# Performance work log

Measured on AMD Instinct MI355X. Metric: run time of the kernel, lower is better.

The kernel has to match this reference:

```python
import jax, jax.numpy as jnp
import numpy as np

N, E, B = 100000, 1600000, 128
F_E, F_X, F_U, H = 128, 128, 128, 64
F_U_OUT = 128


def setup_inputs() -> dict:
    key = jax.random.key(0)
    ks = jax.random.split(key, 16)
    s = lambda fan_in: 1.0 / np.sqrt(fan_in)
    inp = {
        "x": jax.random.normal(ks[0], (N, F_X), jnp.float32),
        "e": jax.random.normal(ks[1], (E, F_E), jnp.float32),
        "u": jax.random.normal(ks[2], (B, F_U), jnp.float32),
        "edge_index": jax.random.randint(ks[3], (2, E), 0, N, jnp.int64),
        "batch": jnp.sort(jax.random.randint(ks[4], (N,), 0, B, jnp.int64)),
        # attention projection params
        "Wk_e": jax.random.uniform(ks[5], (F_E, H), jnp.float32, -s(F_E), s(F_E)),
        "bk_e": jnp.zeros((H,), jnp.float32),
        "Wq_e": jax.random.uniform(ks[6], (F_U, H), jnp.float32, -s(F_U), s(F_U)),
        "bq_e": jnp.zeros((H,), jnp.float32),
        "Wk_x": jax.random.uniform(ks[7], (F_X, H), jnp.float32, -s(F_X), s(F_X)),
        "bk_x": jnp.zeros((H,), jnp.float32),
        "Wq_x": jax.random.uniform(ks[8], (F_U, H), jnp.float32, -s(F_U), s(F_U)),
        "bq_x": jnp.zeros((H,), jnp.float32),
        # phi_u (model_fn = single Linear)
        "Wu": jax.random.uniform(ks[9], (F_E + F_X + F_U, F_U_OUT), jnp.float32,
                                  -s(F_E + F_X + F_U), s(F_E + F_X + F_U)),
        "bu": jnp.zeros((F_U_OUT,), jnp.float32),
    }
    return inp


def reference(x, e, u, edge_index, batch,
              Wk_e, bk_e, Wq_e, bq_e, Wk_x, bk_x, Wq_x, bq_x, Wu, bu):
    num_graphs = u.shape[0]
    src = edge_index[0]
    e_batch = batch[src]                       # [E] graph id per edge

    # edge attention: sigmoid(<k_e, q_e>) per edge, then scatter-add per graph
    k = e @ Wk_e + bk_e                        # [E, H]
    q = (u @ Wq_e + bq_e)[e_batch]             # [E, H] gather
    a_e = jax.nn.sigmoid(jnp.sum(k * q, axis=-1, keepdims=True))  # [E, 1]
    e_agg = jax.ops.segment_sum(a_e * e, e_batch, num_segments=num_graphs)  # [B, F_E]

    # node attention
    kx = x @ Wk_x + bk_x                       # [N, H]
    qx = (u @ Wq_x + bq_x)[batch]              # [N, H] gather
    a_x = jax.nn.sigmoid(jnp.sum(kx * qx, axis=-1, keepdims=True))  # [N, 1]
    x_agg = jax.ops.segment_sum(a_x * x, batch, num_segments=num_graphs)  # [B, F_X]

    out = jnp.concatenate([x_agg, e_agg, u], axis=1)  # [B, F_X+F_E+F_U]
    return out @ Wu + bu                        # [B, F_U_OUT]
```

## Files before the change

kernel.cpp:

```cpp
#include <hip/hip_runtime.h>
#include <hip/hip_bf16.h>


#define FDIM 128
#define BGRAPH 128
#define HDIM 64
#define SLICES 16
#define CAP 16384
#define CURSOR_STRIDE 16
#define SC_THREADS 512
#define SC_ITEMS 16

typedef float vf4 __attribute__((ext_vector_type(4)));

__device__ inline vf4 ldnt4(const float* p) {
    return __builtin_nontemporal_load(reinterpret_cast<const vf4*>(p));
}

__global__ __launch_bounds__(SC_THREADS) void prep_kernel(
    const int* __restrict__ src, const int* __restrict__ batch,
    int* __restrict__ cursor,
    int* __restrict__ order,
    float* __restrict__ e_agg,
    const float* __restrict__ u,
    const float* __restrict__ Wk_e, const float* __restrict__ bk_e,
    const float* __restrict__ Wq_e, const float* __restrict__ bq_e,
    const float* __restrict__ Wk_x, const float* __restrict__ bk_x,
    const float* __restrict__ Wq_x, const float* __restrict__ bq_x,
    float* __restrict__ v_e, float* __restrict__ v_x,
    float* __restrict__ c_e, float* __restrict__ c_x,
    int E, int nb_edge)
{
    const int t = threadIdx.x;

    if (blockIdx.x < nb_edge) {
        __shared__ int lh[BGRAPH];
        __shared__ int s_base[BGRAPH];
        if (t < BGRAPH) lh[t] = 0;
        __syncthreads();

        const int base0 = blockIdx.x * SC_THREADS * SC_ITEMS;
        int gv[SC_ITEMS], rv[SC_ITEMS];
#pragma unroll
        for (int k = 0; k < SC_ITEMS; ++k) {
            const int i = base0 + k * SC_THREADS + t;
            if (i < E) {
                const int g = batch[__builtin_nontemporal_load(src + i)];
                gv[k] = g;
                rv[k] = atomicAdd(&lh[g], 1);
            } else {
                gv[k] = -1; rv[k] = 0;
            }
        }
        __syncthreads();
        if (t < BGRAPH) {
            const int n = lh[t];
            const int b = (n > 0) ? atomicAdd(&cursor[t * CURSOR_STRIDE], n) : 0;
            s_base[t] = t * CAP + b;
        }
        __syncthreads();
#pragma unroll
        for (int k = 0; k < SC_ITEMS; ++k) {
            const int i = base0 + k * SC_THREADS + t;
            if (gv[k] >= 0) order[s_base[gv[k]] + rv[k]] = i;
        }
    } else {
        const int g = blockIdx.x - nb_edge;
        __shared__ float su[FDIM];
        __shared__ float sqe[HDIM];
        __shared__ float sqx[HDIM];

        if (t < FDIM) {
            e_agg[g * FDIM + t] = 0.f;
            su[t] = u[g * FDIM + t];
        }
        __syncthreads();

        if (t < HDIM) {
            float acc = bq_e[t];
            for (int f = 0; f < FDIM; ++f) acc += su[f] * Wq_e[f * HDIM + t];
            sqe[t] = acc;
        } else if (t < 2 * HDIM) {
            const int h = t - HDIM;
            float acc = bq_x[h];
            for (int f = 0; f < FDIM; ++f) acc += su[f] * Wq_x[f * HDIM + h];
            sqx[h] = acc;
        }
        __syncthreads();

        if (t < FDIM) {
            float acce = 0.f, accx = 0.f;
            for (int h = 0; h < HDIM; ++h) {
                acce += Wk_e[t * HDIM + h] * sqe[h];
                accx += Wk_x[t * HDIM + h] * sqx[h];
            }
            v_e[g * FDIM + t] = acce;
            v_x[g * FDIM + t] = accx;
        }
        if (t == 0) {
            float ce = 0.f, cx = 0.f;
            for (int h = 0; h < HDIM; ++h) { ce += bk_e[h] * sqe[h]; cx += bk_x[h] * sqx[h]; }
            c_e[g] = ce;
            c_x[g] = cx;
        }
    }
}

__global__ __launch_bounds__(1024) void agg_kernel(
    const float* __restrict__ e,
    const float* __restrict__ x,
    const int*   __restrict__ order,
    const int*   __restrict__ cursor,
    const int*   __restrict__ batch,
    const float* __restrict__ v_e, const float* __restrict__ c_e,
    const float* __restrict__ v_x, const float* __restrict__ c_x,
    float* __restrict__ e_agg,
    float* __restrict__ x_agg,
    int N)
{
    const int tid  = threadIdx.x;
    const int hidx = tid >> 5;
    const int hl   = tid & 31;
    __shared__ float s_red[32][FDIM];

    const int NEDGE = BGRAPH * SLICES;
    if (blockIdx.x < NEDGE) {
        const int g = blockIdx.x / SLICES;
        const int s = blockIdx.x % SLICES;
        const int len = cursor[g * CURSOR_STRIDE];
        const int lo = g * CAP;
        const int chunk = (len + SLICES - 1) / SLICES;
        const int clo = lo + s * chunk;
        const int chi = min(clo + chunk, lo + len);

        const vf4 fv = *reinterpret_cast<const vf4*>(v_e + g * FDIM + 4 * hl);
        const float cg = c_e[g];

        vf4 acc = (vf4)(0.f);

        int pos = clo + hidx;
        int j1 = 0, j2 = 0;
        vf4 fe0 = (vf4)(0.f), fe1 = (vf4)(0.f);
        if (pos < chi) {
            const int j0 = order[pos];
            fe0 = ldnt4(e + (size_t)j0 * FDIM + 4 * hl);
        }
        if (pos + 32 < chi) {
            j1 = order[pos + 32];
            fe1 = ldnt4(e + (size_t)j1 * FDIM + 4 * hl);
        }
        if (pos + 64 < chi) j2 = order[pos + 64];

        for (; pos < chi; pos += 32) {
            const int j3 = (pos + 96 < chi) ? order[pos + 96] : 0;
            vf4 fe2 = (vf4)(0.f);
            if (pos + 64 < chi)
                fe2 = ldnt4(e + (size_t)j2 * FDIM + 4 * hl);

            float d = fe0.x * fv.x + fe0.y * fv.y + fe0.z * fv.z + fe0.w * fv.w;
            d += __shfl_xor(d, 1);
            d += __shfl_xor(d, 2);
            d += __shfl_xor(d, 4);
            d += __shfl_xor(d, 8);
            d += __shfl_xor(d, 16);
            const float a = 1.f / (1.f + __expf(-(d + cg)));
            acc.x += a * fe0.x; acc.y += a * fe0.y; acc.z += a * fe0.z; acc.w += a * fe0.w;

            fe0 = fe1; fe1 = fe2; j2 = j3;
        }

        s_red[hidx][4 * hl + 0] = acc.x;
        s_red[hidx][4 * hl + 1] = acc.y;
        s_red[hidx][4 * hl + 2] = acc.z;
        s_red[hidx][4 * hl + 3] = acc.w;
        __syncthreads();

        if (tid < FDIM) {
            float ssum = 0.f;
#pragma unroll
            for (int k = 0; k < 32; ++k) ssum += s_red[k][tid];
            unsafeAtomicAdd(&e_agg[g * FDIM + tid], ssum);
        }
    } else {
        const int g = blockIdx.x - NEDGE;
        int lo = 0, hi = N;
        while (lo < hi) { int mid = (lo + hi) >> 1; if (batch[mid] < g) lo = mid + 1; else hi = mid; }
        const int start = lo;
        hi = N;
        while (lo < hi) { int mid = (lo + hi) >> 1; if (batch[mid] < g + 1) lo = mid + 1; else hi = mid; }
        const int end = lo;

        const vf4 fv = *reinterpret_cast<const vf4*>(v_x + g * FDIM + 4 * hl);
        const float cg = c_x[g];

        vf4 acc = (vf4)(0.f);
        for (int row = start + hidx; row < end; row += 32) {
            const vf4 fe = ldnt4(x + (size_t)row * FDIM + 4 * hl);
            float d = fe.x * fv.x + fe.y * fv.y + fe.z * fv.z + fe.w * fv.w;
            d += __shfl_xor(d, 1);
            d += __shfl_xor(d, 2);
            d += __shfl_xor(d, 4);
            d += __shfl_xor(d, 8);
            d += __shfl_xor(d, 16);
            const float a = 1.f / (1.f + __expf(-(d + cg)));
            acc.x += a * fe.x; acc.y += a * fe.y; acc.z += a * fe.z; acc.w += a * fe.w;
        }

        s_red[hidx][4 * hl + 0] = acc.x;
        s_red[hidx][4 * hl + 1] = acc.y;
        s_red[hidx][4 * hl + 2] = acc.z;
        s_red[hidx][4 * hl + 3] = acc.w;
        __syncthreads();

        if (tid < FDIM) {
            float ssum = 0.f;
#pragma unroll
            for (int k = 0; k < 32; ++k) ssum += s_red[k][tid];
            x_agg[g * FDIM + tid] = ssum;
        }
    }
}

__global__ __launch_bounds__(128) void final_kernel(
    const float* __restrict__ x_agg, const float* __restrict__ e_agg,
    const float* __restrict__ u,
    const float* __restrict__ Wu, const float* __restrict__ bu,
    float* __restrict__ out)
{
    const int g = blockIdx.x;
    const int o = threadIdx.x;
    __shared__ float cat[3 * FDIM];
    cat[o]            = x_agg[g * FDIM + o];
    cat[FDIM + o]     = e_agg[g * FDIM + o];
    cat[2 * FDIM + o] = u[g * FDIM + o];
    __syncthreads();

    float acc = bu[o];
#pragma unroll 8
    for (int r = 0; r < 3 * FDIM; ++r) acc += cat[r] * Wu[r * FDIM + o];
    out[g * FDIM + o] = acc;
}

extern "C" void kernel_launch(void* const* d_in, const int* in_sizes, int n_in,
                              void* d_out, int out_size, void* d_ws, size_t ws_size,
                              hipStream_t stream) {
    const float* x          = (const float*)d_in[0];
    const float* e          = (const float*)d_in[1];
    const float* u          = (const float*)d_in[2];
    const int*   edge_index = (const int*)d_in[3];
    const int*   batch      = (const int*)d_in[4];
    const float* Wk_e = (const float*)d_in[5];
    const float* bk_e = (const float*)d_in[6];
    const float* Wq_e = (const float*)d_in[7];
    const float* bq_e = (const float*)d_in[8];
    const float* Wk_x = (const float*)d_in[9];
    const float* bk_x = (const float*)d_in[10];
    const float* Wq_x = (const float*)d_in[11];
    const float* bq_x = (const float*)d_in[12];
    const float* Wu   = (const float*)d_in[13];
    const float* bu   = (const float*)d_in[14];

    const int N = in_sizes[4];
    const int E = in_sizes[3] / 2;
    const int* src = edge_index;

    float* ws    = (float*)d_ws;
    float* v_e   = ws;
    float* v_x   = v_e + BGRAPH * FDIM;
    float* c_e   = v_x + BGRAPH * FDIM;
    float* c_x   = c_e + BGRAPH;
    float* e_agg = c_x + BGRAPH;
    float* x_agg = e_agg + BGRAPH * FDIM;
    int*   cursor = (int*)(x_agg + BGRAPH * FDIM);
    int*   order  = cursor + BGRAPH * CURSOR_STRIDE;

    hipMemsetAsync(cursor, 0, BGRAPH * CURSOR_STRIDE * sizeof(int), stream);

    const int nb_edge = (E + SC_THREADS * SC_ITEMS - 1) / (SC_THREADS * SC_ITEMS);
    prep_kernel<<<nb_edge + BGRAPH, SC_THREADS, 0, stream>>>(
        src, batch, cursor, order, e_agg,
        u, Wk_e, bk_e, Wq_e, bq_e, Wk_x, bk_x, Wq_x, bq_x,
        v_e, v_x, c_e, c_x, E, nb_edge);

    agg_kernel<<<BGRAPH * SLICES + BGRAPH, 1024, 0, stream>>>(
        e, x, order, cursor, batch, v_e, c_e, v_x, c_x, e_agg, x_agg, N);

    final_kernel<<<BGRAPH, 128, 0, stream>>>(
        x_agg, e_agg, u, Wu, bu, (float*)d_out);
}
```

Baseline: 221.2 us.

## Move node attention aggregation into prep kernel's per-graph blocks

The per-graph node attention reduction is moved from the aggregation kernel into the per-graph blocks of the prep kernel. Those blocks now keep the projected query vector and bias term in shared memory and use 512 threads, i.e. 16 rows at a time. The node work can then overlap with the edge bucketing phase instead of competing with the edge gather, and the v_x and c_x global round trips go away. The edge aggregation kernel now handles only edges and gains a min-blocks launch bound. The risk is that the per-graph prep blocks become long-running tail blocks with half the per-block parallelism.

```diff
diff --git a/kernel.cpp b/kernel.cpp
--- a/kernel.cpp
+++ b/kernel.cpp
@@ -22,14 +22,15 @@
     int* __restrict__ cursor,
     int* __restrict__ order,
     float* __restrict__ e_agg,
+    float* __restrict__ x_agg,
+    const float* __restrict__ x,
     const float* __restrict__ u,
     const float* __restrict__ Wk_e, const float* __restrict__ bk_e,
     const float* __restrict__ Wq_e, const float* __restrict__ bq_e,
     const float* __restrict__ Wk_x, const float* __restrict__ bk_x,
     const float* __restrict__ Wq_x, const float* __restrict__ bq_x,
-    float* __restrict__ v_e, float* __restrict__ v_x,
-    float* __restrict__ c_e, float* __restrict__ c_x,
-    int E, int nb_edge)
+    float* __restrict__ v_e, float* __restrict__ c_e,
+    int E, int N, int nb_edge)
 {
     const int t = threadIdx.x;
 
@@ -69,6 +70,8 @@
         __shared__ float su[FDIM];
         __shared__ float sqe[HDIM];
         __shared__ float sqx[HDIM];
+        __shared__ float s_vx[FDIM];
+        __shared__ float s_cx;
 
         if (t < FDIM) {
             e_agg[g * FDIM + t] = 0.f;
@@ -95,94 +98,16 @@
                 accx += Wk_x[t * HDIM + h] * sqx[h];
             }
             v_e[g * FDIM + t] = acce;
-            v_x[g * FDIM + t] = accx;
+            s_vx[t] = accx;
         }
         if (t == 0) {
             float ce = 0.f, cx = 0.f;
             for (int h = 0; h < HDIM; ++h) { ce += bk_e[h] * sqe[h]; cx += bk_x[h] * sqx[h]; }
             c_e[g] = ce;
-            c_x[g] = cx;
-        }
-    }
-}
-
-__global__ __launch_bounds__(1024) void agg_kernel(
-    const float* __restrict__ e,
-    const float* __restrict__ x,
-    const int*   __restrict__ order,
-    const int*   __restrict__ cursor,
-    const int*   __restrict__ batch,
-    const float* __restrict__ v_e, const float* __restrict__ c_e,
-    const float* __restrict__ v_x, const float* __restrict__ c_x,
-    float* __restrict__ e_agg,
-    float* __restrict__ x_agg,
-    int N)
-{
-    const int tid  = threadIdx.x;
-    const int hidx = tid >> 5;
-    const int hl   = tid & 31;
-    __shared__ float s_red[32][FDIM];
-
-    const int NEDGE = BGRAPH * SLICES;
-    if (blockIdx.x < NEDGE) {
-        const int g = blockIdx.x / SLICES;
-        const int s = blockIdx.x % SLICES;
-        const int len = cursor[g * CURSOR_STRIDE];
-        const int lo = g * CAP;
-        const int chunk = (len + SLICES - 1) / SLICES;
-        const int clo = lo + s * chunk;
-        const int chi = min(clo + chunk, lo + len);
-
-        const vf4 fv = *reinterpret_cast<const vf4*>(v_e + g * FDIM + 4 * hl);
-        const float cg = c_e[g];
-
-        vf4 acc = (vf4)(0.f);
-
-        int pos = clo + hidx;
-        int j1 = 0, j2 = 0;
-        vf4 fe0 = (vf4)(0.f), fe1 = (vf4)(0.f);
-        if (pos < chi) {
-            const int j0 = order[pos];
-            fe0 = ldnt4(e + (size_t)j0 * FDIM + 4 * hl);
-        }
-        if (pos + 32 < chi) {
-            j1 = order[pos + 32];
-            fe1 = ldnt4(e + (size_t)j1 * FDIM + 4 * hl);
-        }
-        if (pos + 64 < chi) j2 = order[pos + 64];
-
-        for (; pos < chi; pos += 32) {
-            const int j3 = (pos + 96 < chi) ? order[pos + 96] : 0;
-            vf4 fe2 = (vf4)(0.f);
-            if (pos + 64 < chi)
-                fe2 = ldnt4(e + (size_t)j2 * FDIM + 4 * hl);
-
-            float d = fe0.x * fv.x + fe0.y * fv.y + fe0.z * fv.z + fe0.w * fv.w;
-            d += __shfl_xor(d, 1);
-            d += __shfl_xor(d, 2);
-            d += __shfl_xor(d, 4);
-            d += __shfl_xor(d, 8);
-            d += __shfl_xor(d, 16);
-            const float a = 1.f / (1.f + __expf(-(d + cg)));
-            acc.x += a * fe0.x; acc.y += a * fe0.y; acc.z += a * fe0.z; acc.w += a * fe0.w;
-
-            fe0 = fe1; fe1 = fe2; j2 = j3;
-        }
-
-        s_red[hidx][4 * hl + 0] = acc.x;
-        s_red[hidx][4 * hl + 1] = acc.y;
-        s_red[hidx][4 * hl + 2] = acc.z;
-        s_red[hidx][4 * hl + 3] = acc.w;
-        __syncthreads();
-
-        if (tid < FDIM) {
-            float ssum = 0.f;
-#pragma unroll
-            for (int k = 0; k < 32; ++k) ssum += s_red[k][tid];
-            unsafeAtomicAdd(&e_agg[g * FDIM + tid], ssum);
-        }
-    } else {
-        const int g = blockIdx.x - NEDGE;
+            s_cx = cx;
+        }
+        __syncthreads();
+
         int lo = 0, hi = N;
         while (lo < hi) { int mid = (lo + hi) >> 1; if (batch[mid] < g) lo = mid + 1; else hi = mid; }
         const int start = lo;
@@ -190,11 +115,13 @@
         while (lo < hi) { int mid = (lo + hi) >> 1; if (batch[mid] < g + 1) lo = mid + 1; else hi = mid; }
         const int end = lo;
 
-        const vf4 fv = *reinterpret_cast<const vf4*>(v_x + g * FDIM + 4 * hl);
-        const float cg = c_x[g];
+        const int hidx = t >> 5;
+        const int hl   = t & 31;
+        const vf4 fv = *reinterpret_cast<const vf4*>(&s_vx[4 * hl]);
+        const float cg = s_cx;
 
         vf4 acc = (vf4)(0.f);
-        for (int row = start + hidx; row < end; row += 32) {
+        for (int row = start + hidx; row < end; row += 16) {
             const vf4 fe = ldnt4(x + (size_t)row * FDIM + 4 * hl);
             float d = fe.x * fv.x + fe.y * fv.y + fe.z * fv.z + fe.w * fv.w;
             d += __shfl_xor(d, 1);
@@ -206,18 +133,89 @@
             acc.x += a * fe.x; acc.y += a * fe.y; acc.z += a * fe.z; acc.w += a * fe.w;
         }
 
+        __shared__ float s_red[16][FDIM];
         s_red[hidx][4 * hl + 0] = acc.x;
         s_red[hidx][4 * hl + 1] = acc.y;
         s_red[hidx][4 * hl + 2] = acc.z;
         s_red[hidx][4 * hl + 3] = acc.w;
         __syncthreads();
 
-        if (tid < FDIM) {
+        if (t < FDIM) {
             float ssum = 0.f;
 #pragma unroll
-            for (int k = 0; k < 32; ++k) ssum += s_red[k][tid];
-            x_agg[g * FDIM + tid] = ssum;
-        }
+            for (int k = 0; k < 16; ++k) ssum += s_red[k][t];
+            x_agg[g * FDIM + t] = ssum;
+        }
+    }
+}
+
+__global__ __launch_bounds__(1024, 8) void agg_kernel(
+    const float* __restrict__ e,
+    const int*   __restrict__ order,
+    const int*   __restrict__ cursor,
+    const float* __restrict__ v_e, const float* __restrict__ c_e,
+    float* __restrict__ e_agg)
+{
+    const int tid  = threadIdx.x;
+    const int hidx = tid >> 5;
+    const int hl   = tid & 31;
+    __shared__ float s_red[32][FDIM];
+
+    const int g = blockIdx.x / SLICES;
+    const int s = blockIdx.x % SLICES;
+    const int len = cursor[g * CURSOR_STRIDE];
+    const int lo = g * CAP;
+    const int chunk = (len + SLICES - 1) / SLICES;
+    const int clo = lo + s * chunk;
+    const int chi = min(clo + chunk, lo + len);
+
+    const vf4 fv = *reinterpret_cast<const vf4*>(v_e + g * FDIM + 4 * hl);
+    const float cg = c_e[g];
+
+    vf4 acc = (vf4)(0.f);
+
+    int pos = clo + hidx;
+    int j1 = 0, j2 = 0;
+    vf4 fe0 = (vf4)(0.f), fe1 = (vf4)(0.f);
+    if (pos < chi) {
+        const int j0 = order[pos];
+        fe0 = ldnt4(e + (size_t)j0 * FDIM + 4 * hl);
+    }
+    if (pos + 32 < chi) {
+        j1 = order[pos + 32];
+        fe1 = ldnt4(e + (size_t)j1 * FDIM + 4 * hl);
+    }
+    if (pos + 64 < chi) j2 = order[pos + 64];
+
+    for (; pos < chi; pos += 32) {
+        const int j3 = (pos + 96 < chi) ? order[pos + 96] : 0;
+        vf4 fe2 = (vf4)(0.f);
+        if (pos + 64 < chi)
+            fe2 = ldnt4(e + (size_t)j2 * FDIM + 4 * hl);
+
+        float d = fe0.x * fv.x + fe0.y * fv.y + fe0.z * fv.z + fe0.w * fv.w;
+        d += __shfl_xor(d, 1);
+        d += __shfl_xor(d, 2);
+        d += __shfl_xor(d, 4);
+        d += __shfl_xor(d, 8);
+        d += __shfl_xor(d, 16);
+        const float a = 1.f / (1.f + __expf(-(d + cg)));
+        acc.x += a * fe0.x; acc.y += a * fe0.y; acc.z += a * fe0.z; acc.w += a * fe0.w;
+
+        fe0 = fe1; fe1 = fe2; j2 = j3;
+    }
+
+    s_red[hidx][4 * hl + 0] = acc.x;
+    s_red[hidx][4 * hl + 1] = acc.y;
+    s_red[hidx][4 * hl + 2] = acc.z;
+    s_red[hidx][4 * hl + 3] = acc.w;
+    __syncthreads();
+
+    if (tid < FDIM) {
+        float ssum = 0.f;
+#pragma unroll
+        for (int k = 0; k < 32; ++k) ssum += s_red[k][tid];
+        unsafeAtomicAdd(&e_agg[g * FDIM + tid], ssum);
     }
 }
 
@@ -266,10 +264,8 @@
 
     float* ws    = (float*)d_ws;
     float* v_e   = ws;
-    float* v_x   = v_e + BGRAPH * FDIM;
-    float* c_e   = v_x + BGRAPH * FDIM;
-    float* c_x   = c_e + BGRAPH;
-    float* e_agg = c_x + BGRAPH;
+    float* c_e   = v_e + BGRAPH * FDIM;
+    float* e_agg = c_e + BGRAPH;
     float* x_agg = e_agg + BGRAPH * FDIM;
     int*   cursor = (int*)(x_agg + BGRAPH * FDIM);
     int*   order  = cursor + BGRAPH * CURSOR_STRIDE;
@@ -278,12 +274,12 @@
 
     const int nb_edge = (E + SC_THREADS * SC_ITEMS - 1) / (SC_THREADS * SC_ITEMS);
     prep_kernel<<<nb_edge + BGRAPH, SC_THREADS, 0, stream>>>(
-        src, batch, cursor, order, e_agg,
+        src, batch, cursor, order, e_agg, x_agg, x,
         u, Wk_e, bk_e, Wq_e, bq_e, Wk_x, bk_x, Wq_x, bq_x,
-        v_e, v_x, c_e, c_x, E, nb_edge);
-
-    agg_kernel<<<BGRAPH * SLICES + BGRAPH, 1024, 0, stream>>>(
-        e, x, order, cursor, batch, v_e, c_e, v_x, c_x, e_agg, x_agg, N);
+        v_e, c_e, E, N, nb_edge);
+
+    agg_kernel<<<BGRAPH * SLICES, 1024, 0, stream>>>(
+        e, order, cursor, v_e, c_e, e_agg);
 
     final_kernel<<<BGRAPH, 128, 0, stream>>>(
         x_agg, e_agg, u, Wu, bu, (float*)d_out);
```

Result: faster. 213.1 us (-3.7%).
